# Kernel optimization log

Hardware: AMD Instinct MI355X
Metric: run time of the kernel (lower is better)

## Reference

```python
import jax, jax.numpy as jnp
import numpy as np

B, T, D, H = 8, 4096, 512, 512


def log_g(x):
    # log of g(x) where g(x) = relu(x) + 0.5 for x >= 0, sigmoid(x) for x < 0
    return jnp.where(x >= 0, jnp.log(jax.nn.relu(x) + 0.5), -jax.nn.softplus(-x))


def setup_inputs() -> dict:
    key = jax.random.key(0)
    kx, kh0, kwz, kbz, kwh, kbh = jax.random.split(key, 6)
    s = 1.0 / np.sqrt(D)
    return {
        "x": jax.random.normal(kx, (B, T, D), dtype=jnp.float32),
        "h_0": jax.random.uniform(kh0, (B, H), dtype=jnp.float32),
        "Wz": jax.random.uniform(kwz, (H, D), dtype=jnp.float32, minval=-s, maxval=s),
        "bz": jax.random.uniform(kbz, (H,), dtype=jnp.float32, minval=-s, maxval=s),
        "Wh": jax.random.uniform(kwh, (H, D), dtype=jnp.float32, minval=-s, maxval=s),
        "bh": jax.random.uniform(kbh, (H,), dtype=jnp.float32, minval=-s, maxval=s),
    }


def parallel_scan_log(log_coeffs, log_values):
    # log_coeffs: (B, T, H), log_values: (B, T+1, H)
    a_star = jnp.cumsum(jnp.pad(log_coeffs, ((0, 0), (1, 0), (0, 0))), axis=1)  # (B, T+1, H)
    log_h = a_star + jax.lax.cumlogsumexp(log_values - a_star, axis=1)
    return jnp.exp(log_h)  # (B, T+1, H)


def reference(x, h_0, Wz, bz, Wh, bh):
    k = jnp.einsum('btd,hd->bth', x, Wz) + bz                # (B, T, H)
    log_z = -jax.nn.softplus(-k)                              # log sigmoid(k)
    log_coeffs = -jax.nn.softplus(k)                          # log (1 - sigmoid(k))
    log_h0 = log_g(h_0)[:, None, :]                           # (B, 1, H)
    log_tilde_h = log_g(jnp.einsum('btd,hd->bth', x, Wh) + bh)
    vals = jnp.concatenate([log_h0, log_z + log_tilde_h], axis=1)  # (B, T+1, H)
    h = parallel_scan_log(log_coeffs, vals)
    return h[:, -x.shape[1]:, :]                              # (B, T, H)
```

## Files before the change

kernel.cpp:

```cpp
#include <hip/hip_runtime.h>
#include <math.h>

#define Bq 8
#define Tq 4096
#define Dq 512
#define Hq 512
#define Mq (Bq * Tq)
#define NC 64
#define CL 64

typedef unsigned short ushort_t;
typedef unsigned int uint_t;
typedef __bf16 bf16x8 __attribute__((ext_vector_type(8)));
typedef float f32x4 __attribute__((ext_vector_type(4)));

__device__ __forceinline__ ushort_t f2bf(float f) {
    unsigned int u = __float_as_uint(f);
    unsigned int r = u + 0x7fffu + ((u >> 16) & 1u);
    return (ushort_t)(r >> 16);
}

__device__ __forceinline__ void gload16(const void* g, void* l) {
    __builtin_amdgcn_global_load_lds(
        (const __attribute__((address_space(1))) void*)g,
        (__attribute__((address_space(3))) void*)l, 16, 0, 0);
}

__device__ __forceinline__ void gates(uint_t w, float& c, float& v) {
    float k  = __uint_as_float((w & 0xffffu) << 16);
    float th = __uint_as_float(w & 0xffff0000u);
    float ek = __expf(k);
    c = 1.0f / (1.0f + ek);
    float z = 1.0f - c;
    float g = (th >= 0.0f) ? (th + 0.5f) : (1.0f / (1.0f + __expf(-th)));
    v = z * g;
}

__global__ __launch_bounds__(256)
void convert_all(const float* __restrict__ x, const float* __restrict__ Wz,
                 const float* __restrict__ Wh, ushort_t* __restrict__ dst) {
    size_t i8 = ((size_t)blockIdx.x * 256 + threadIdx.x) * 8;
    const size_t XN = (size_t)Mq * Dq;
    const size_t WN = (size_t)Hq * Dq;
    const float* src; size_t off;
    if (i8 < XN)            { src = x;  off = i8; }
    else if (i8 < XN + WN)  { src = Wz; off = i8 - XN; }
    else                    { src = Wh; off = i8 - XN - WN; }
    float4 a = *reinterpret_cast<const float4*>(src + off);
    float4 b = *reinterpret_cast<const float4*>(src + off + 4);
    uint4 o;
    o.x = (uint_t)f2bf(a.x) | ((uint_t)f2bf(a.y) << 16);
    o.y = (uint_t)f2bf(a.z) | ((uint_t)f2bf(a.w) << 16);
    o.z = (uint_t)f2bf(b.x) | ((uint_t)f2bf(b.y) << 16);
    o.w = (uint_t)f2bf(b.z) | ((uint_t)f2bf(b.w) << 16);
    *reinterpret_cast<uint4*>(dst + i8) = o;
}

__global__ __launch_bounds__(256, 2)
void gemm_fused(const ushort_t* __restrict__ xb, const ushort_t* __restrict__ wb,
                const float* __restrict__ bz, const float* __restrict__ bh,
                uint_t* __restrict__ kvout, float2* __restrict__ chAW) {
    __shared__ __align__(16) ushort_t smem[3 * 128 * 64];
    ushort_t* As  = smem;
    ushort_t* Bzs = smem + 128 * 64;
    ushort_t* Bhs = smem + 2 * 128 * 64;

    const int tid  = threadIdx.x;
    const int lane = tid & 63;
    const int wave = tid >> 6;
    const int wm = (wave >> 1) * 64;
    const int wn = (wave & 1) * 64;
    const int mBase = blockIdx.x * 128;
    const int nBase = blockIdx.y * 128;
    const ushort_t* Wzb = wb;
    const ushort_t* Whb = wb + (size_t)Hq * Dq;

    f32x4 zero = {0.f, 0.f, 0.f, 0.f};
    f32x4 accz[4][4], acch[4][4];
#pragma unroll
    for (int i = 0; i < 4; ++i)
#pragma unroll
        for (int j = 0; j < 4; ++j) { accz[i][j] = zero; acch[i][j] = zero; }

    const int rowInW = lane >> 3;
    const int ccG = (lane & 7) ^ rowInW;
    const int swz = lane & 7;

    for (int k0 = 0; k0 < Dq; k0 += 64) {
#pragma unroll
        for (int j = 0; j < 4; ++j) {
            const int rseg = j * 4 + wave;
            const int row  = rseg * 8 + rowInW;
            const size_t gcol = (size_t)(k0 + ccG * 8);
            gload16(xb  + (size_t)(mBase + row) * Dq + gcol, &As [rseg * 512]);
            gload16(Wzb + (size_t)(nBase + row) * Dq + gcol, &Bzs[rseg * 512]);
            gload16(Whb + (size_t)(nBase + row) * Dq + gcol, &Bhs[rseg * 512]);
        }
        __syncthreads();

#pragma unroll
        for (int ks = 0; ks < 2; ++ks) {
            const int cc = ks * 4 + (lane >> 4);
            const int sc = cc ^ swz;
            bf16x8 af[4], bzf[4], bhf[4];
#pragma unroll
            for (int i = 0; i < 4; ++i) {
                int rowA = wm + i * 16 + (lane & 15);
                af[i] = *reinterpret_cast<const bf16x8*>(&As[rowA * 64 + sc * 8]);
            }
#pragma unroll
            for (int i = 0; i < 4; ++i) {
                int rowB = wn + i * 16 + (lane & 15);
                bzf[i] = *reinterpret_cast<const bf16x8*>(&Bzs[rowB * 64 + sc * 8]);
                bhf[i] = *reinterpret_cast<const bf16x8*>(&Bhs[rowB * 64 + sc * 8]);
            }
#pragma unroll
            for (int mi = 0; mi < 4; ++mi)
#pragma unroll
                for (int ni = 0; ni < 4; ++ni) {
                    accz[mi][ni] = __builtin_amdgcn_mfma_f32_16x16x32_bf16(
                        af[mi], bzf[ni], accz[mi][ni], 0, 0, 0);
                    acch[mi][ni] = __builtin_amdgcn_mfma_f32_16x16x32_bf16(
                        af[mi], bhf[ni], acch[mi][ni], 0, 0, 0);
                }
        }
        __syncthreads();
    }

    const int colL = lane & 15;
    const int quad = lane >> 4;
    float2* sb = reinterpret_cast<float2*>(smem) + wave * 1024;

#pragma unroll
    for (int ni = 0; ni < 4; ++ni) {
        int h = nBase + wn + ni * 16 + colL;
        float bzv = bz[h];
        float bhv = bh[h];
#pragma unroll
        for (int mi = 0; mi < 4; ++mi) {
            float A = 1.f, W = 0.f;
#pragma unroll
            for (int r = 0; r < 4; ++r) {
                int bt = mBase + wm + mi * 16 + quad * 4 + r;
                float kf  = accz[mi][ni][r] + bzv;
                float thf = acch[mi][ni][r] + bhv;
                uint_t word = (uint_t)f2bf(kf) | ((uint_t)f2bf(thf) << 16);
                kvout[(size_t)bt * Hq + h] = word;
                float c, v;
                gates(word, c, v);
                W = fmaf(c, W, v);
                A *= c;
            }
            sb[(mi * 4 + quad) * 64 + ni * 16 + colL] = make_float2(A, W);
        }
    }
    __syncthreads();
    {
        float A = 1.f, W = 0.f;
#pragma unroll
        for (int s = 0; s < 16; ++s) {
            float2 aw = sb[s * 64 + lane];
            W = fmaf(aw.x, W, aw.y);
            A *= aw.x;
        }
        int g = blockIdx.x * 2 + (wm >> 6);
        int h = nBase + wn + lane;
        chAW[(size_t)g * Hq + h] = make_float2(A, W);
    }
}

__global__ __launch_bounds__(256)
void scan_combine(const float* __restrict__ h0, const float2* __restrict__ chAW,
                  float* __restrict__ hstart) {
    int idx = blockIdx.x * 256 + threadIdx.x;
    int b = idx >> 9;
    int h = idx & (Hq - 1);
    float x0 = h0[idx];
    float r = (x0 >= 0.f) ? (x0 + 0.5f) : (1.f / (1.f + __expf(-x0)));
    const float2* p = chAW + (size_t)b * NC * Hq + h;
    for (int c0 = 0; c0 < NC; c0 += 16) {
        float2 aw[16];
#pragma unroll
        for (int j = 0; j < 16; ++j) aw[j] = p[(size_t)(c0 + j) * Hq];
#pragma unroll
        for (int j = 0; j < 16; ++j) {
            hstart[((size_t)b * NC + c0 + j) * Hq + h] = r;
            r = fmaf(aw[j].x, r, aw[j].y);
        }
    }
}

__global__ __launch_bounds__(256)
void scan_final(const uint_t* kv, const float* __restrict__ hstart, float* out) {
    const int b = blockIdx.x >> 6;
    const int chunk = blockIdx.x & 63;
    const int h2 = threadIdx.x;
    float2 hs = reinterpret_cast<const float2*>(hstart)[(size_t)blockIdx.x * (Hq / 2) + h2];
    float r0 = hs.x, r1 = hs.y;
    const uint2* kv2 = reinterpret_cast<const uint2*>(kv);
    float2* out2 = reinterpret_cast<float2*>(out);
    size_t base = ((size_t)b * Tq + (size_t)chunk * CL) * (Hq / 2) + h2;

    uint2 w[8];
#pragma unroll
    for (int j = 0; j < 8; ++j) w[j] = kv2[base + (size_t)j * (Hq / 2)];

    for (int bt = 0; bt < 8; ++bt) {
        uint2 wn[8];
        if (bt < 7) {
#pragma unroll
            for (int j = 0; j < 8; ++j)
                wn[j] = kv2[base + (size_t)((bt + 1) * 8 + j) * (Hq / 2)];
        }
#pragma unroll
        for (int j = 0; j < 8; ++j) {
            float c0, v0, c1, v1;
            gates(w[j].x, c0, v0);
            gates(w[j].y, c1, v1);
            r0 = fmaf(c0, r0, v0);
            r1 = fmaf(c1, r1, v1);
            out2[base + (size_t)(bt * 8 + j) * (Hq / 2)] = make_float2(r0, r1);
        }
#pragma unroll
        for (int j = 0; j < 8; ++j) w[j] = wn[j];
    }
}

extern "C" void kernel_launch(void* const* d_in, const int* in_sizes, int n_in,
                              void* d_out, int out_size, void* d_ws, size_t ws_size,
                              hipStream_t stream) {
    const float* x  = (const float*)d_in[0];
    const float* h0 = (const float*)d_in[1];
    const float* Wz = (const float*)d_in[2];
    const float* bz = (const float*)d_in[3];
    const float* Wh = (const float*)d_in[4];
    const float* bh = (const float*)d_in[5];
    float* out = (float*)d_out;

    char* ws = (char*)d_ws;
    ushort_t* xb = (ushort_t*)ws;
    ushort_t* wb = xb + (size_t)Mq * Dq;
    float2* chAW = (float2*)(wb + 2 * (size_t)Hq * Dq);
    float* hstart = (float*)((char*)chAW + (size_t)Bq * NC * Hq * sizeof(float2));
    uint_t* kv = (uint_t*)d_out;

    const int totalConv = (Mq * Dq + 2 * Hq * Dq) / (256 * 8);
    convert_all<<<dim3(totalConv), dim3(256), 0, stream>>>(x, Wz, Wh, xb);
    gemm_fused<<<dim3(Mq / 128, Hq / 128), dim3(256), 0, stream>>>(xb, wb, bz, bh, kv, chAW);
    scan_combine<<<dim3((Bq * Hq) / 256), dim3(256), 0, stream>>>(h0, chAW, hstart);
    scan_final<<<dim3(Bq * NC), dim3(256), 0, stream>>>(kv, hstart, out);
}
```

Before: 199.7 us.

## Move chunk reduction out of GEMM epilogue into cooperative scan kernel

The per-chunk (A,W) reduction is removed from the GEMM epilogue, which now only writes packed bf16 k/h pairs. A new cooperative kernel recomputes the chunk summaries by re-reading kv, runs the cross-chunk combine, and then the final scan, with grid-wide syncs between phases. A fallback runs three separate kernels if the cooperative launch fails. This trades a lighter GEMM epilogue and fewer launches for an extra full read of the kv buffer, two grid barriers, and a phase B in which only 8 blocks do work while the rest wait.

New measurement: 497.6 us. +149.2%, slower.

```diff
diff --git a/kernel.cpp b/kernel.cpp
--- a/kernel.cpp
+++ b/kernel.cpp
@@ -1,4 +1,5 @@
 #include <hip/hip_runtime.h>
+#include <hip/hip_cooperative_groups.h>
 #include <math.h>
 
 #define Bq 8
@@ -59,11 +60,10 @@
 __global__ __launch_bounds__(256, 2)
 void gemm_fused(const ushort_t* __restrict__ xb, const ushort_t* __restrict__ wb,
                 const float* __restrict__ bz, const float* __restrict__ bh,
-                uint_t* __restrict__ kvout, float2* __restrict__ chAW) {
-    __shared__ __align__(16) ushort_t smem[3 * 128 * 64];
-    ushort_t* As  = smem;
-    ushort_t* Bzs = smem + 128 * 64;
-    ushort_t* Bhs = smem + 2 * 128 * 64;
+                uint_t* __restrict__ kvout) {
+    __shared__ __align__(16) ushort_t As [128 * 64];
+    __shared__ __align__(16) ushort_t Bzs[128 * 64];
+    __shared__ __align__(16) ushort_t Bhs[128 * 64];
 
     const int tid  = threadIdx.x;
     const int lane = tid & 63;
@@ -128,102 +128,117 @@
     }
 
     const int colL = lane & 15;
-    const int quad = lane >> 4;
-    float2* sb = reinterpret_cast<float2*>(smem) + wave * 1024;
-
-#pragma unroll
-    for (int ni = 0; ni < 4; ++ni) {
-        int h = nBase + wn + ni * 16 + colL;
-        float bzv = bz[h];
-        float bhv = bh[h];
-#pragma unroll
-        for (int mi = 0; mi < 4; ++mi) {
-            float A = 1.f, W = 0.f;
+    const int rowQ = (lane >> 4) * 4;
+#pragma unroll
+    for (int mi = 0; mi < 4; ++mi) {
+#pragma unroll
+        for (int ni = 0; ni < 4; ++ni) {
+            int h = nBase + wn + ni * 16 + colL;
+            float bzv = bz[h];
+            float bhv = bh[h];
 #pragma unroll
             for (int r = 0; r < 4; ++r) {
-                int bt = mBase + wm + mi * 16 + quad * 4 + r;
+                int bt = mBase + wm + mi * 16 + rowQ + r;
                 float kf  = accz[mi][ni][r] + bzv;
                 float thf = acch[mi][ni][r] + bhv;
-                uint_t word = (uint_t)f2bf(kf) | ((uint_t)f2bf(thf) << 16);
-                kvout[(size_t)bt * Hq + h] = word;
-                float c, v;
-                gates(word, c, v);
-                W = fmaf(c, W, v);
-                A *= c;
+                kvout[(size_t)bt * Hq + h] =
+                    (uint_t)f2bf(kf) | ((uint_t)f2bf(thf) << 16);
             }
-            sb[(mi * 4 + quad) * 64 + ni * 16 + colL] = make_float2(A, W);
-        }
-    }
-    __syncthreads();
-    {
-        float A = 1.f, W = 0.f;
-#pragma unroll
-        for (int s = 0; s < 16; ++s) {
-            float2 aw = sb[s * 64 + lane];
-            W = fmaf(aw.x, W, aw.y);
-            A *= aw.x;
-        }
-        int g = blockIdx.x * 2 + (wm >> 6);
-        int h = nBase + wn + lane;
-        chAW[(size_t)g * Hq + h] = make_float2(A, W);
-    }
-}
-
-__global__ __launch_bounds__(256)
-void scan_combine(const float* __restrict__ h0, const float2* __restrict__ chAW,
-                  float* __restrict__ hstart) {
-    int idx = blockIdx.x * 256 + threadIdx.x;
-    int b = idx >> 9;
-    int h = idx & (Hq - 1);
-    float x0 = h0[idx];
+        }
+    }
+}
+
+__device__ __forceinline__ void phaseA(const uint_t* kv, float2* chAW, int blk, int h) {
+    const int b = blk >> 6, c = blk & 63;
+    size_t base = ((size_t)b * Tq + (size_t)c * CL) * Hq + h;
+    float A = 1.f, W = 0.f;
+    for (int t0 = 0; t0 < CL; t0 += 16) {
+        uint_t w[16];
+#pragma unroll
+        for (int j = 0; j < 16; ++j) w[j] = kv[base + (size_t)(t0 + j) * Hq];
+#pragma unroll
+        for (int j = 0; j < 16; ++j) {
+            float cc, vv;
+            gates(w[j], cc, vv);
+            W = fmaf(cc, W, vv);
+            A *= cc;
+        }
+    }
+    chAW[(size_t)blk * Hq + h] = make_float2(A, W);
+}
+
+__device__ __forceinline__ void phaseB(const float* h0, const float2* chAW,
+                                       float* hstart, int b, int h) {
+    float x0 = h0[b * Hq + h];
     float r = (x0 >= 0.f) ? (x0 + 0.5f) : (1.f / (1.f + __expf(-x0)));
     const float2* p = chAW + (size_t)b * NC * Hq + h;
+    float* q = hstart + (size_t)b * NC * Hq + h;
     for (int c0 = 0; c0 < NC; c0 += 16) {
         float2 aw[16];
 #pragma unroll
         for (int j = 0; j < 16; ++j) aw[j] = p[(size_t)(c0 + j) * Hq];
 #pragma unroll
         for (int j = 0; j < 16; ++j) {
-            hstart[((size_t)b * NC + c0 + j) * Hq + h] = r;
+            q[(size_t)(c0 + j) * Hq] = r;
             r = fmaf(aw[j].x, r, aw[j].y);
         }
     }
 }
 
-__global__ __launch_bounds__(256)
-void scan_final(const uint_t* kv, const float* __restrict__ hstart, float* out) {
-    const int b = blockIdx.x >> 6;
-    const int chunk = blockIdx.x & 63;
-    const int h2 = threadIdx.x;
-    float2 hs = reinterpret_cast<const float2*>(hstart)[(size_t)blockIdx.x * (Hq / 2) + h2];
-    float r0 = hs.x, r1 = hs.y;
-    const uint2* kv2 = reinterpret_cast<const uint2*>(kv);
-    float2* out2 = reinterpret_cast<float2*>(out);
-    size_t base = ((size_t)b * Tq + (size_t)chunk * CL) * (Hq / 2) + h2;
-
-    uint2 w[8];
-#pragma unroll
-    for (int j = 0; j < 8; ++j) w[j] = kv2[base + (size_t)j * (Hq / 2)];
-
+__device__ __forceinline__ void phaseC(const uint_t* kv, const float* hstart,
+                                       float* out, int blk, int h) {
+    const int b = blk >> 6, c = blk & 63;
+    float r = hstart[(size_t)blk * Hq + h];
+    size_t base = ((size_t)b * Tq + (size_t)c * CL) * Hq + h;
+    uint_t w[8];
+#pragma unroll
+    for (int j = 0; j < 8; ++j) w[j] = kv[base + (size_t)j * Hq];
     for (int bt = 0; bt < 8; ++bt) {
-        uint2 wn[8];
+        uint_t wn[8];
         if (bt < 7) {
 #pragma unroll
             for (int j = 0; j < 8; ++j)
-                wn[j] = kv2[base + (size_t)((bt + 1) * 8 + j) * (Hq / 2)];
+                wn[j] = kv[base + (size_t)((bt + 1) * 8 + j) * Hq];
         }
 #pragma unroll
         for (int j = 0; j < 8; ++j) {
-            float c0, v0, c1, v1;
-            gates(w[j].x, c0, v0);
-            gates(w[j].y, c1, v1);
-            r0 = fmaf(c0, r0, v0);
-            r1 = fmaf(c1, r1, v1);
-            out2[base + (size_t)(bt * 8 + j) * (Hq / 2)] = make_float2(r0, r1);
+            float cc, vv;
+            gates(w[j], cc, vv);
+            r = fmaf(cc, r, vv);
+            out[base + (size_t)(bt * 8 + j) * Hq] = r;
         }
 #pragma unroll
         for (int j = 0; j < 8; ++j) w[j] = wn[j];
     }
+}
+
+__global__ __launch_bounds__(512, 4)
+void scan_coop(const float* __restrict__ h0, float2* chAW, float* hstart, float* out) {
+    const int blk = blockIdx.x;
+    const int h = threadIdx.x;
+    const uint_t* kv = reinterpret_cast<const uint_t*>(out);
+    phaseA(kv, chAW, blk, h);
+    __threadfence();
+    cooperative_groups::this_grid().sync();
+    if ((blk & 63) == 0) phaseB(h0, chAW, hstart, blk >> 6, h);
+    __threadfence();
+    cooperative_groups::this_grid().sync();
+    phaseC(kv, hstart, out, blk, h);
+}
+
+__global__ __launch_bounds__(512)
+void k_phaseA(const uint_t* __restrict__ kv, float2* __restrict__ chAW) {
+    phaseA(kv, chAW, blockIdx.x, threadIdx.x);
+}
+__global__ __launch_bounds__(512)
+void k_phaseB(const float* __restrict__ h0, const float2* __restrict__ chAW,
+              float* __restrict__ hstart) {
+    int idx = blockIdx.x * 512 + threadIdx.x;
+    phaseB(h0, chAW, hstart, idx >> 9, idx & (Hq - 1));
+}
+__global__ __launch_bounds__(512)
+void k_phaseC(const uint_t* kv, const float* __restrict__ hstart, float* out) {
+    phaseC(kv, hstart, out, blockIdx.x, threadIdx.x);
 }
 
 extern "C" void kernel_launch(void* const* d_in, const int* in_sizes, int n_in,
@@ -246,7 +261,15 @@
 
     const int totalConv = (Mq * Dq + 2 * Hq * Dq) / (256 * 8);
     convert_all<<<dim3(totalConv), dim3(256), 0, stream>>>(x, Wz, Wh, xb);
-    gemm_fused<<<dim3(Mq / 128, Hq / 128), dim3(256), 0, stream>>>(xb, wb, bz, bh, kv, chAW);
-    scan_combine<<<dim3((Bq * Hq) / 256), dim3(256), 0, stream>>>(h0, chAW, hstart);
-    scan_final<<<dim3(Bq * NC), dim3(256), 0, stream>>>(kv, hstart, out);
-}
+    gemm_fused<<<dim3(Mq / 128, Hq / 128), dim3(256), 0, stream>>>(xb, wb, bz, bh, kv);
+
+    const float* h0a = h0; float2* chAWa = chAW; float* hstarta = hstart; float* outa = out;
+    void* args[] = {(void*)&h0a, (void*)&chAWa, (void*)&hstarta, (void*)&outa};
+    hipError_t e = hipLaunchCooperativeKernel(reinterpret_cast<void*>(scan_coop),
+                                              dim3(Bq * NC), dim3(512), args, 0, stream);
+    if (e != hipSuccess) {
+        k_phaseA<<<dim3(Bq * NC), dim3(512), 0, stream>>>(kv, chAW);
+        k_phaseB<<<dim3((Bq * Hq) / 512), dim3(512), 0, stream>>>(h0, chAW, hstart);
+        k_phaseC<<<dim3(Bq * NC), dim3(512), 0, stream>>>(kv, hstart, out);
+    }
+}
```
